# Optimization experiments

Measured on AMD Instinct MI355X. Metric: run time of the kernel, lower is better.

The kernel has to match this reference:

```python
import jax, jax.numpy as jnp
import numpy as np

N_CLI, N_AGG, E, D, L = 100000, 1000, 1600000, 128, 3


def setup_inputs() -> dict:
    key = jax.random.key(0)
    ks = jax.random.split(key, 16)
    inp = {
        'x_clients': jax.random.normal(ks[0], (N_CLI, D), jnp.float32),
        'x_agg': jax.random.normal(ks[1], (N_AGG, D), jnp.float32),
        'c2a_src': jax.random.randint(ks[2], (E,), 0, N_CLI, jnp.int32),
        'c2a_dst': jax.random.randint(ks[3], (E,), 0, N_AGG, jnp.int32),
        'a2c_src': jax.random.randint(ks[4], (E,), 0, N_AGG, jnp.int32),
        'a2c_dst': jax.random.randint(ks[5], (E,), 0, N_CLI, jnp.int32),
    }
    s = 1.0 / np.sqrt(D)
    # stacked per-layer SAGE params for each edge type: W_l (on aggregated msg), W_r (on dst), b
    inp['Wl_c2a'] = jax.random.uniform(ks[6], (L, D, D), jnp.float32, -s, s)
    inp['Wr_c2a'] = jax.random.uniform(ks[7], (L, D, D), jnp.float32, -s, s)
    inp['b_c2a'] = jax.random.uniform(ks[8], (L, D), jnp.float32, -s, s)
    inp['Wl_a2c'] = jax.random.uniform(ks[9], (L, D, D), jnp.float32, -s, s)
    inp['Wr_a2c'] = jax.random.uniform(ks[10], (L, D, D), jnp.float32, -s, s)
    inp['b_a2c'] = jax.random.uniform(ks[11], (L, D), jnp.float32, -s, s)
    inp['W_lin'] = jax.random.uniform(ks[12], (D, 1), jnp.float32, -s, s)
    inp['b_lin'] = jax.random.uniform(ks[13], (1,), jnp.float32, -s, s)
    return inp


def _sage(x_src, x_dst, src, dst, Wl, Wr, b, n_dst):
    # mean aggregation of gathered source features onto dst nodes
    msg = x_src[src]                                        # [E, D]
    summed = jax.ops.segment_sum(msg, dst, num_segments=n_dst)
    cnt = jax.ops.segment_sum(jnp.ones((src.shape[0], 1), x_src.dtype), dst, num_segments=n_dst)
    mean = summed / jnp.maximum(cnt, 1.0)
    return mean @ Wl + x_dst @ Wr + b


def _leaky(x):
    return jnp.where(x >= 0, x, 0.1 * x)


def reference(x_clients, x_agg, c2a_src, c2a_dst, a2c_src, a2c_dst,
              Wl_c2a, Wr_c2a, b_c2a, Wl_a2c, Wr_a2c, b_a2c, W_lin, b_lin):
    xc, xa = x_clients, x_agg
    for l in range(L):
        new_a = _sage(xc, xa, c2a_src, c2a_dst, Wl_c2a[l], Wr_c2a[l], b_c2a[l], N_AGG)
        new_c = _sage(xa, xc, a2c_src, a2c_dst, Wl_a2c[l], Wr_a2c[l], b_a2c[l], N_CLI)
        xa, xc = _leaky(new_a), _leaky(new_c)
    return (xc @ W_lin + b_lin).squeeze(1)
```

## Files before the change

### kernel.cpp

```cpp
#include <hip/hip_runtime.h>

#define D      128
#define NCLI   100000
#define NAGG   1000
#define NLAYER 3
#define NBKT   782
#define NRNG   8
#define NBIN   (NAGG * NRNG)
#define RMAGIC 343598u
#define NHIST  512
#define NCVTX  (NCLI * D / 4 / 256)
#define NCVTW  ((NLAYER * D * D + 255) / 256)
#define NROWT  (NCLI / 32)

typedef short bf16x8 __attribute__((ext_vector_type(8)));
typedef float f32x16 __attribute__((ext_vector_type(16)));

static __device__ __forceinline__ float leaky(float x) { return x >= 0.f ? x : 0.1f * x; }

static __device__ __forceinline__ unsigned bf16_rn(float f) {
    unsigned u = __float_as_uint(f);
    return (u + 0x7fffu + ((u >> 16) & 1u)) >> 16;
}
static __device__ __forceinline__ float bf_val(unsigned h) { return __uint_as_float(h << 16); }
static __device__ __forceinline__ unsigned pack_bf2(float lo, float hi) {
    return bf16_rn(lo) | (bf16_rn(hi) << 16);
}
static __device__ __forceinline__ float bf_lo(unsigned v) { return __uint_as_float(v << 16); }
static __device__ __forceinline__ float bf_hi(unsigned v) { return __uint_as_float(v & 0xffff0000u); }

__global__ __launch_bounds__(256) void prep(const int* __restrict__ c2a_src,
                                            const int* __restrict__ c2a_dst,
                                            const int* __restrict__ a2c_dst, int E,
                                            int* __restrict__ cnt_ar, int* __restrict__ bcnt,
                                            const float4* __restrict__ X4,
                                            uint2* __restrict__ xhi, uint2* __restrict__ xlo,
                                            const float* __restrict__ W,
                                            unsigned short* __restrict__ Wt) {
    __shared__ int h[NBIN + NBKT];
    int bid = blockIdx.x;
    if (bid < NHIST) {
        for (int i = threadIdx.x; i < NBIN + NBKT; i += 256) h[i] = 0;
        __syncthreads();
        int stride = NHIST * 256;
        for (int e = bid * 256 + threadIdx.x; e < E; e += stride) {
            int s = c2a_src[e];
            int bin = c2a_dst[e] * NRNG + (int)__umulhi((unsigned)s, RMAGIC);
            atomicAdd(&h[bin], 1);
            atomicAdd(&h[NBIN + (a2c_dst[e] >> 7)], 1);
        }
        __syncthreads();
        for (int i = threadIdx.x; i < NBIN; i += 256)
            if (h[i]) atomicAdd(&cnt_ar[i], h[i]);
        for (int i = threadIdx.x; i < NBKT; i += 256)
            if (h[NBIN + i]) atomicAdd(&bcnt[i], h[NBIN + i]);
    } else if (bid < NHIST + NCVTX) {
        int t = (bid - NHIST) * 256 + threadIdx.x;
        float4 f = X4[t];
        unsigned h0 = bf16_rn(f.x), h1 = bf16_rn(f.y), h2 = bf16_rn(f.z), h3 = bf16_rn(f.w);
        xhi[t] = make_uint2(h0 | (h1 << 16), h2 | (h3 << 16));
        xlo[t] = make_uint2(pack_bf2(f.x - bf_val(h0), f.y - bf_val(h1)),
                            pack_bf2(f.z - bf_val(h2), f.w - bf_val(h3)));
    } else {
        int idx = (bid - NHIST - NCVTX) * 256 + threadIdx.x;
        if (idx >= NLAYER * D * D) return;
        int layer = idx >> 14, rem = idx & (D * D - 1);
        int k = rem >> 7, n = rem & 127;
        float w = W[layer * D * D + k * D + n];
        unsigned hh = bf16_rn(w);
        unsigned short* base = Wt + layer * 2 * D * D;
        base[n * D + k] = (unsigned short)hh;
        base[D * D + n * D + k] = (unsigned short)bf16_rn(w - bf_val(hh));
    }
}

__global__ void scan_both(const int* __restrict__ cnt_ar, int* __restrict__ rp_ar,
                          int* __restrict__ cur_ar, const int* __restrict__ bcnt,
                          int* __restrict__ brp, int* __restrict__ bcur) {
    __shared__ int sh[1024];
    int t = threadIdx.x;
    if (blockIdx.x == 0) {
        int v[8];
        int s = 0;
#pragma unroll
        for (int j = 0; j < 8; j++) {
            int idx = t * 8 + j;
            v[j] = (idx < NBIN) ? cnt_ar[idx] : 0;
            s += v[j];
        }
        sh[t] = s;
        __syncthreads();
        for (int off = 1; off < 1024; off <<= 1) {
            int x = (t >= off) ? sh[t - off] : 0;
            __syncthreads();
            sh[t] += x;
            __syncthreads();
        }
        int run = sh[t] - s;
#pragma unroll
        for (int j = 0; j < 8; j++) {
            int idx = t * 8 + j;
            if (idx < NBIN) {
                rp_ar[idx] = run;
                cur_ar[idx] = run;
            }
            run += v[j];
        }
        if (t == 1023) rp_ar[NBIN] = sh[1023];
    } else {
        int v = (t < NBKT) ? bcnt[t] : 0;
        sh[t] = v;
        __syncthreads();
        for (int off = 1; off < 1024; off <<= 1) {
            int x = (t >= off) ? sh[t - off] : 0;
            __syncthreads();
            sh[t] += x;
            __syncthreads();
        }
        if (t == 0) { brp[0] = 0; bcur[0] = 0; }
        if (t < NBKT) {
            brp[t + 1] = sh[t];
            if (t + 1 < NBKT) bcur[t + 1] = sh[t];
        }
    }
}

__global__ __launch_bounds__(1024) void scatter_both(const int* __restrict__ c2a_src,
                                                     const int* __restrict__ c2a_dst,
                                                     const int* __restrict__ a2c_src,
                                                     const int* __restrict__ a2c_dst, int E,
                                                     int* __restrict__ cur_ar,
                                                     int* __restrict__ col_c2a,
                                                     int* __restrict__ bcur,
                                                     int* __restrict__ sorted1) {
    __shared__ int sbuf[2 * NBIN];
    int tid = threadIdx.x;
    if (blockIdx.x < 256) {
        int* h = sbuf;
        int* base = sbuf + NBIN;
        int chunk = (E + 255) / 256;
        int e0 = blockIdx.x * chunk;
        int e1 = min(E, e0 + chunk);
        for (int i = tid; i < NBIN; i += 1024) h[i] = 0;
        __syncthreads();
        for (int e = e0 + tid; e < e1; e += 1024) {
            int s = c2a_src[e];
            atomicAdd(&h[c2a_dst[e] * NRNG + (int)__umulhi((unsigned)s, RMAGIC)], 1);
        }
        __syncthreads();
        for (int i = tid; i < NBIN; i += 1024) {
            int c = h[i];
            base[i] = c ? atomicAdd(&cur_ar[i], c) : 0;
        }
        __syncthreads();
        for (int e = e0 + tid; e < e1; e += 1024) {
            int s = c2a_src[e];
            int bin = c2a_dst[e] * NRNG + (int)__umulhi((unsigned)s, RMAGIC);
            int pos = atomicAdd(&base[bin], 1);
            col_c2a[pos] = s;
        }
    } else {
        int* h = sbuf;
        int* base = sbuf + NBKT;
        int bid = blockIdx.x - 256;
        int chunk = (E + 255) / 256;
        int e0 = bid * chunk;
        int e1 = min(E, e0 + chunk);
        for (int i = tid; i < NBKT; i += 1024) h[i] = 0;
        __syncthreads();
        for (int e = e0 + tid; e < e1; e += 1024) atomicAdd(&h[a2c_dst[e] >> 7], 1);
        __syncthreads();
        for (int i = tid; i < NBKT; i += 1024) {
            int c = h[i];
            base[i] = c ? atomicAdd(&bcur[i], c) : 0;
        }
        __syncthreads();
        for (int e = e0 + tid; e < e1; e += 1024) {
            int d = a2c_dst[e];
            int pos = atomicAdd(&base[d >> 7], 1);
            sorted1[pos] = ((d & 127) << 10) | a2c_src[e];
        }
    }
}

__global__ __launch_bounds__(512) void bucket_csr(const int* __restrict__ brp,
                                                  const int* __restrict__ sorted1,
                                                  int* __restrict__ rp_c,
                                                  int* __restrict__ col) {
    __shared__ int h[128], cur[128];
    int b = blockIdx.x, tid = threadIdx.x;
    if (tid < 128) h[tid] = 0;
    __syncthreads();
    int beg = brp[b], end = brp[b + 1];
    for (int e = beg + tid; e < end; e += 512) atomicAdd(&h[sorted1[e] >> 10], 1);
    __syncthreads();
    if (tid < 128) cur[tid] = h[tid];
    __syncthreads();
    for (int off = 1; off < 128; off <<= 1) {
        int x = 0;
        if (tid < 128 && tid >= off) x = cur[tid - off];
        __syncthreads();
        if (tid < 128) cur[tid] += x;
        __syncthreads();
    }
    if (tid < 128) {
        int start = beg + cur[tid] - h[tid];
        int c = b * 128 + tid;
        if (c < NCLI) rp_c[c] = start;
        cur[tid] = start;
    }
    if (b == NBKT - 1 && tid == 0) rp_c[NCLI] = end;
    __syncthreads();
    for (int e = beg + tid; e < end; e += 512) {
        int p = sorted1[e];
        int pos = atomicAdd(&cur[p >> 10], 1);
        col[pos] = p & 1023;
    }
}


__global__ __launch_bounds__(512) void gather_mean(const unsigned* __restrict__ tbl,
                                                   const int* __restrict__ rp_ar,
                                                   const int* __restrict__ col,
                                                   float* __restrict__ psum) {
    __shared__ float part[4][8][D];
    int quad = blockIdx.x >> 3, r = blockIdx.x & 7;
    int tid = threadIdx.x;
    int a = tid >> 7;
    int sub = (tid >> 4) & 7;
    int sl = tid & 15;
    const uint4* tbl4 = (const uint4*)tbl;
    int agg = quad * 4 + a;
    int bin = agg * NRNG + r;
    int beg = rp_ar[bin], end = rp_ar[bin + 1];
    float f0 = 0, f1 = 0, f2 = 0, f3 = 0, f4 = 0, f5 = 0, f6 = 0, f7 = 0;
    int e = beg + sub;
    for (; e + 8 < end; e += 16) {
        int s0 = col[e];
        int s1 = col[e + 8];
        uint4 v0 = tbl4[(s0 << 4) + sl];
        uint4 v1 = tbl4[(s1 << 4) + sl];
        f0 += bf_lo(v0.x); f1 += bf_hi(v0.x); f2 += bf_lo(v0.y); f3 += bf_hi(v0.y);
        f4 += bf_lo(v0.z); f5 += bf_hi(v0.z); f6 += bf_lo(v0.w); f7 += bf_hi(v0.w);
        f0 += bf_lo(v1.x); f1 += bf_hi(v1.x); f2 += bf_lo(v1.y); f3 += bf_hi(v1.y);
        f4 += bf_lo(v1.z); f5 += bf_hi(v1.z); f6 += bf_lo(v1.w); f7 += bf_hi(v1.w);
    }
    if (e < end) {
        int s0 = col[e];
        uint4 v0 = tbl4[(s0 << 4) + sl];
        f0 += bf_lo(v0.x); f1 += bf_hi(v0.x); f2 += bf_lo(v0.y); f3 += bf_hi(v0.y);
        f4 += bf_lo(v0.z); f5 += bf_hi(v0.z); f6 += bf_lo(v0.w); f7 += bf_hi(v0.w);
    }
    float* pr = &part[a][sub][sl * 8];
    pr[0] = f0; pr[1] = f1; pr[2] = f2; pr[3] = f3;
    pr[4] = f4; pr[5] = f5; pr[6] = f6; pr[7] = f7;
    __syncthreads();
    int c = tid & 127;
    float s = 0.f;
#pragma unroll
    for (int g = 0; g < 8; g++) s += part[a][g][c];
    psum[((size_t)agg * NRNG + r) * D + c] = s;
}

__global__ __launch_bounds__(128) void combine_agg(const float* __restrict__ psum,
                                                   const int* __restrict__ rp_ar,
                                                   const float* xa_old,
                                                   const float* __restrict__ Wl_a2c,
                                                   const float* __restrict__ Wl_c2a,
                                                   const float* __restrict__ Wr_c2a,
                                                   const float* __restrict__ b_c2a,
                                                   unsigned short* __restrict__ ya_bf,
                                                   float* xa_out) {
    __shared__ float mr[D], xr[D];
    int i = blockIdx.x, j = threadIdx.x;
    const float* pr = psum + (size_t)i * NRNG * D + j;
    float s = 0.f;
#pragma unroll
    for (int r = 0; r < NRNG; r++) s += pr[r * D];
    int deg = rp_ar[i * NRNG + NRNG] - rp_ar[i * NRNG];
    mr[j] = s / fmaxf((float)deg, 1.f);
    xr[j] = xa_old[i * D + j];
    __syncthreads();
    float accy = 0.f, accn = b_c2a[j];
#pragma unroll 4
    for (int k = 0; k < D; k++) {
        accy += xr[k] * Wl_a2c[k * D + j];
        accn += mr[k] * Wl_c2a[k * D + j] + xr[k] * Wr_c2a[k * D + j];
    }
    ya_bf[i * D + j] = (unsigned short)bf16_rn(accy);
    xa_out[i * D + j] = leaky(accn);
}

__global__ __launch_bounds__(256) void gemm_mfma(const unsigned short* __restrict__ Ahi,
                                                 const unsigned short* __restrict__ Alo,
                                                 const unsigned short* __restrict__ Wt,
                                                 const float* __restrict__ bias,
                                                 float* __restrict__ Y) {
    int tid = threadIdx.x;
    int wave = tid >> 6, lane = tid & 63;
    int cl = lane & 31, kh = lane >> 5;
    int n0 = wave * 32;
    const unsigned short* Wlo = Wt + D * D;
    const unsigned short* wbh = Wt + (size_t)(n0 + cl) * D + kh * 8;
    const unsigned short* wbl = Wlo + (size_t)(n0 + cl) * D + kh * 8;
    bf16x8 bhi[8], blo[8];
#pragma unroll
    for (int kc = 0; kc < 8; kc++) {
        bhi[kc] = *(const bf16x8*)(wbh + kc * 16);
        blo[kc] = *(const bf16x8*)(wbl + kc * 16);
    }
    float bv = bias[n0 + cl];
    for (int r = blockIdx.x; r < NROWT; r += gridDim.x) {
        int m0 = r * 32;
        const unsigned short* ar = Ahi + (size_t)(m0 + cl) * D + kh * 8;
        const unsigned short* al = Alo + (size_t)(m0 + cl) * D + kh * 8;
        bf16x8 ahi[8], alo[8];
#pragma unroll
        for (int kc = 0; kc < 8; kc++) {
            ahi[kc] = *(const bf16x8*)(ar + kc * 16);
            alo[kc] = *(const bf16x8*)(al + kc * 16);
        }
        f32x16 acc;
#pragma unroll
        for (int q = 0; q < 16; q++) acc[q] = bv;
#pragma unroll
        for (int kc = 0; kc < 8; kc++) {
            acc = __builtin_amdgcn_mfma_f32_32x32x16_bf16(ahi[kc], bhi[kc], acc, 0, 0, 0);
            acc = __builtin_amdgcn_mfma_f32_32x32x16_bf16(alo[kc], bhi[kc], acc, 0, 0, 0);
            acc = __builtin_amdgcn_mfma_f32_32x32x16_bf16(ahi[kc], blo[kc], acc, 0, 0, 0);
        }
        float* yb = Y + (size_t)m0 * D + n0 + cl;
#pragma unroll
        for (int reg = 0; reg < 16; reg++) {
            int row = (reg & 3) + 8 * (reg >> 2) + 4 * kh;
            yb[(size_t)row * D] = acc[reg];
        }
    }
}

template <int LAST>
__global__ __launch_bounds__(256) void agg_c_bf(const unsigned* __restrict__ ya,
                                                const int* __restrict__ rowptr,
                                                const int* __restrict__ col,
                                                const float* __restrict__ Y,
                                                unsigned* __restrict__ xhi,
                                                unsigned* __restrict__ xlo,
                                                const float* __restrict__ Wlin,
                                                const float* __restrict__ blin,
                                                float* __restrict__ out, int E) {
    int l = threadIdx.x & 63;
    int gid = blockIdx.x * 4 + (threadIdx.x >> 6);
    if (gid >= NCLI) return;
    int beg = rowptr[gid], end = rowptr[gid + 1];
    float a0 = 0, b0 = 0, a1 = 0, b1 = 0, a2 = 0, b2 = 0, a3 = 0, b3 = 0;
    float a4 = 0, b4 = 0, a5 = 0, b5 = 0, a6 = 0, b6 = 0, a7 = 0, b7 = 0;
    for (int ch = beg; ch < end; ch += 64) {
        int len = min(64, end - ch);
        int ec = col[min(ch + l, E - 1)];
        int j = 0;
        for (; j + 8 <= len; j += 8) {
            int r0 = __shfl(ec, j + 0), r1 = __shfl(ec, j + 1);
            int r2 = __shfl(ec, j + 2), r3 = __shfl(ec, j + 3);
            int r4 = __shfl(ec, j + 4), r5 = __shfl(ec, j + 5);
            int r6 = __shfl(ec, j + 6), r7 = __shfl(ec, j + 7);
            unsigned v0 = ya[(r0 << 6) + l];
            unsigned v1 = ya[(r1 << 6) + l];
            unsigned v2 = ya[(r2 << 6) + l];
            unsigned v3 = ya[(r3 << 6) + l];
            unsigned v4 = ya[(r4 << 6) + l];
            unsigned v5 = ya[(r5 << 6) + l];
            unsigned v6 = ya[(r6 << 6) + l];
            unsigned v7 = ya[(r7 << 6) + l];
            a0 += bf_lo(v0); b0 += bf_hi(v0);
            a1 += bf_lo(v1); b1 += bf_hi(v1);
            a2 += bf_lo(v2); b2 += bf_hi(v2);
            a3 += bf_lo(v3); b3 += bf_hi(v3);
            a4 += bf_lo(v4); b4 += bf_hi(v4);
            a5 += bf_lo(v5); b5 += bf_hi(v5);
            a6 += bf_lo(v6); b6 += bf_hi(v6);
            a7 += bf_lo(v7); b7 += bf_hi(v7);
        }
        for (; j < len; j++) {
            int r = __shfl(ec, j);
            unsigned v = ya[(r << 6) + l];
            a0 += bf_lo(v); b0 += bf_hi(v);
        }
    }
    float sx = ((a0 + a1) + (a2 + a3)) + ((a4 + a5) + (a6 + a7));
    float sy = ((b0 + b1) + (b2 + b3)) + ((b4 + b5) + (b6 + b7));
    float inv = 1.f / fmaxf((float)(end - beg), 1.f);
    float2 yv = *(const float2*)&Y[(size_t)gid * D + 2 * l];
    float r0 = leaky(yv.x + sx * inv);
    float r1 = leaky(yv.y + sy * inv);
    if (LAST) {
        float2 w = *(const float2*)&Wlin[2 * l];
        float v = r0 * w.x + r1 * w.y;
#pragma unroll
        for (int off = 32; off > 0; off >>= 1) v += __shfl_down(v, off);
        if (l == 0) out[gid] = v + blin[0];
    } else {
        unsigned h0 = bf16_rn(r0), h1 = bf16_rn(r1);
        xhi[(gid << 6) + l] = h0 | (h1 << 16);
        xlo[(gid << 6) + l] = pack_bf2(r0 - bf_val(h0), r1 - bf_val(h1));
    }
}

extern "C" void kernel_launch(void* const* d_in, const int* in_sizes, int n_in,
                              void* d_out, int out_size, void* d_ws, size_t ws_size,
                              hipStream_t stream) {
    const float* x_clients = (const float*)d_in[0];
    const float* x_agg     = (const float*)d_in[1];
    const int*   c2a_src   = (const int*)d_in[2];
    const int*   c2a_dst   = (const int*)d_in[3];
    const int*   a2c_src   = (const int*)d_in[4];
    const int*   a2c_dst   = (const int*)d_in[5];
    const float* Wl_c2a    = (const float*)d_in[6];
    const float* Wr_c2a    = (const float*)d_in[7];
    const float* b_c2a     = (const float*)d_in[8];
    const float* Wl_a2c    = (const float*)d_in[9];
    const float* Wr_a2c    = (const float*)d_in[10];
    const float* b_a2c     = (const float*)d_in[11];
    const float* W_lin     = (const float*)d_in[12];
    const float* b_lin     = (const float*)d_in[13];
    float* out = (float*)d_out;
    const int E = in_sizes[2];

    char* p = (char*)d_ws;
    auto alloc = [&](size_t bytes) {
        char* r = p;
        p += (bytes + 255) & ~(size_t)255;
        return r;
    };
    float*    Yb    = (float*)alloc(sizeof(float) * NCLI * D);
    unsigned* xc_hi = (unsigned*)alloc(sizeof(unsigned) * NCLI * 64);
    unsigned* xc_lo = (unsigned*)alloc(sizeof(unsigned) * NCLI * 64);
    float*    xa    = (float*)alloc(sizeof(float) * NAGG * D);
    unsigned short* ya_bf = (unsigned short*)alloc(sizeof(unsigned short) * NAGG * D);
    unsigned short* Wt = (unsigned short*)alloc(sizeof(unsigned short) * NLAYER * 2 * D * D);
    float* psum  = (float*)alloc(sizeof(float) * NAGG * NRNG * D);
    int* cnt_ar = (int*)alloc(sizeof(int) * (NBIN + NBKT));
    int* bcnt  = cnt_ar + NBIN;
    int* rp_ar = (int*)alloc(sizeof(int) * (NBIN + 1));
    int* cur_ar = (int*)alloc(sizeof(int) * NBIN);
    int* brp   = (int*)alloc(sizeof(int) * (NBKT + 1));
    int* bcur  = (int*)alloc(sizeof(int) * NBKT);
    int* rp_c  = (int*)alloc(sizeof(int) * (NCLI + 1));
    int* col_c2a = (int*)alloc(sizeof(int) * E);
    int* col_a2c = (int*)alloc(sizeof(int) * E);
    int* sorted1 = (int*)Yb;

    hipMemsetAsync(cnt_ar, 0, sizeof(int) * (NBIN + NBKT), stream);

    prep<<<NHIST + NCVTX + NCVTW, 256, 0, stream>>>(c2a_src, c2a_dst, a2c_dst, E, cnt_ar, bcnt,
                                                    (const float4*)x_clients,
                                                    (uint2*)xc_hi, (uint2*)xc_lo,
                                                    Wr_a2c, Wt);
    scan_both<<<2, 1024, 0, stream>>>(cnt_ar, rp_ar, cur_ar, bcnt, brp, bcur);
    scatter_both<<<512, 1024, 0, stream>>>(c2a_src, c2a_dst, a2c_src, a2c_dst, E,
                                           cur_ar, col_c2a, bcur, sorted1);
    bucket_csr<<<NBKT, 512, 0, stream>>>(brp, sorted1, rp_c, col_a2c);

    const float* xa_old = x_agg;
    for (int l = 0; l < NLAYER; l++) {
        gather_mean<<<(NAGG / 4) * NRNG, 512, 0, stream>>>(xc_hi, rp_ar, col_c2a, psum);
        combine_agg<<<NAGG, 128, 0, stream>>>(psum, rp_ar, xa_old,
                                              Wl_a2c + l * D * D, Wl_c2a + l * D * D,
                                              Wr_c2a + l * D * D, b_c2a + l * D, ya_bf, xa);
        gemm_mfma<<<625, 256, 0, stream>>>(
            (const unsigned short*)xc_hi, (const unsigned short*)xc_lo,
            Wt + l * 2 * D * D, b_a2c + l * D, Yb);
        if (l < NLAYER - 1) {
            agg_c_bf<0><<<(NCLI + 3) / 4, 256, 0, stream>>>((const unsigned*)ya_bf, rp_c, col_a2c,
                                                            Yb, xc_hi, xc_lo, nullptr, nullptr,
                                                            nullptr, E);
        } else {
            agg_c_bf<1><<<(NCLI + 3) / 4, 256, 0, stream>>>((const unsigned*)ya_bf, rp_c, col_a2c,
                                                            Yb, nullptr, nullptr, W_lin, b_lin,
                                                            out, E);
        }
        xa_old = xa;
    }
}
```

Measured before the change: 633.8 us.

## Build c2a CSR with two-pass radix scatter, range-major bins

Reorders the c2a bin layout to range-major (range * NAGG + agg). CSR construction becomes a two-pass scatter: first a wave-ballot partition of edges into 8 source ranges, then a per-range scatter by destination using small shared histograms. This replaces the single scatter over 8000 bins, which needed large shared memory and gave poor locality, and folds the a2c bucket CSR pass into the second kernel. The cost is an extra pass over a packed intermediate buffer placed in Yb, plus an 8-term degree sum in combine_agg.

```diff
diff --git a/kernel.cpp b/kernel.cpp
--- a/kernel.cpp
+++ b/kernel.cpp
@@ -45,7 +45,7 @@
         int stride = NHIST * 256;
         for (int e = bid * 256 + threadIdx.x; e < E; e += stride) {
             int s = c2a_src[e];
-            int bin = c2a_dst[e] * NRNG + (int)__umulhi((unsigned)s, RMAGIC);
+            int bin = (int)__umulhi((unsigned)s, RMAGIC) * NAGG + c2a_dst[e];
             atomicAdd(&h[bin], 1);
             atomicAdd(&h[NBIN + (a2c_dst[e] >> 7)], 1);
         }
@@ -75,7 +75,8 @@
 }
 
 __global__ void scan_both(const int* __restrict__ cnt_ar, int* __restrict__ rp_ar,
-                          int* __restrict__ cur_ar, const int* __restrict__ bcnt,
+                          int* __restrict__ cur_ar, int* __restrict__ cur_r8,
+                          const int* __restrict__ bcnt,
                           int* __restrict__ brp, int* __restrict__ bcur) {
     __shared__ int sh[1024];
     int t = threadIdx.x;
@@ -103,6 +104,7 @@
             if (idx < NBIN) {
                 rp_ar[idx] = run;
                 cur_ar[idx] = run;
+                if ((idx % NAGG) == 0) cur_r8[idx / NAGG] = run;
             }
             run += v[j];
         }
@@ -125,44 +127,61 @@
     }
 }
 
-__global__ __launch_bounds__(1024) void scatter_both(const int* __restrict__ c2a_src,
-                                                     const int* __restrict__ c2a_dst,
-                                                     const int* __restrict__ a2c_src,
-                                                     const int* __restrict__ a2c_dst, int E,
-                                                     int* __restrict__ cur_ar,
-                                                     int* __restrict__ col_c2a,
-                                                     int* __restrict__ bcur,
-                                                     int* __restrict__ sorted1) {
-    __shared__ int sbuf[2 * NBIN];
+__global__ __launch_bounds__(1024) void scatter1(const int* __restrict__ c2a_src,
+                                                 const int* __restrict__ c2a_dst,
+                                                 const int* __restrict__ a2c_src,
+                                                 const int* __restrict__ a2c_dst, int E,
+                                                 int* __restrict__ cur_r8,
+                                                 int* __restrict__ sorted_c2a,
+                                                 int* __restrict__ bcur,
+                                                 int* __restrict__ sorted1) {
+    __shared__ int sbuf[2 * NBKT];
     int tid = threadIdx.x;
-    if (blockIdx.x < 256) {
+    if (blockIdx.x < 64) {
         int* h = sbuf;
-        int* base = sbuf + NBIN;
-        int chunk = (E + 255) / 256;
+        int* base = sbuf + 8;
+        int chunk = (E + 63) / 64;
         int e0 = blockIdx.x * chunk;
         int e1 = min(E, e0 + chunk);
-        for (int i = tid; i < NBIN; i += 1024) h[i] = 0;
-        __syncthreads();
-        for (int e = e0 + tid; e < e1; e += 1024) {
-            int s = c2a_src[e];
-            atomicAdd(&h[c2a_dst[e] * NRNG + (int)__umulhi((unsigned)s, RMAGIC)], 1);
-        }
-        __syncthreads();
-        for (int i = tid; i < NBIN; i += 1024) {
-            int c = h[i];
-            base[i] = c ? atomicAdd(&cur_ar[i], c) : 0;
-        }
-        __syncthreads();
-        for (int e = e0 + tid; e < e1; e += 1024) {
-            int s = c2a_src[e];
-            int bin = c2a_dst[e] * NRNG + (int)__umulhi((unsigned)s, RMAGIC);
-            int pos = atomicAdd(&base[bin], 1);
-            col_c2a[pos] = s;
+        int wid = tid >> 6, lane = tid & 63;
+        unsigned long long below = (1ull << lane) - 1;
+        if (tid < 8) h[tid] = 0;
+        __syncthreads();
+        for (int eb = e0 + wid * 64; eb < e1; eb += 16 * 64) {
+            int e = eb + lane;
+            bool valid = e < e1;
+            int s = valid ? c2a_src[e] : 0;
+            int rg = (int)__umulhi((unsigned)s, RMAGIC);
+#pragma unroll
+            for (int r = 0; r < NRNG; r++) {
+                unsigned long long m = __ballot(valid && rg == r);
+                if (lane == r && m) atomicAdd(&h[r], __popcll(m));
+            }
+        }
+        __syncthreads();
+        if (tid < 8) base[tid] = h[tid] ? atomicAdd(&cur_r8[tid], h[tid]) : 0;
+        __syncthreads();
+        for (int eb = e0 + wid * 64; eb < e1; eb += 16 * 64) {
+            int e = eb + lane;
+            bool valid = e < e1;
+            int s = valid ? c2a_src[e] : 0;
+            int dcl = valid ? c2a_dst[e] : 0;
+            int rg = (int)__umulhi((unsigned)s, RMAGIC);
+            unsigned long long mym = 0;
+            int wb = 0;
+#pragma unroll
+            for (int r = 0; r < NRNG; r++) {
+                unsigned long long m = __ballot(valid && rg == r);
+                if (valid && rg == r) mym = m;
+                if (lane == r) wb = m ? atomicAdd(&base[r], __popcll(m)) : 0;
+            }
+            int pb = __shfl(wb, rg);
+            if (valid) sorted_c2a[pb + __popcll(mym & below)] = (dcl << 17) | s;
         }
     } else {
         int* h = sbuf;
         int* base = sbuf + NBKT;
-        int bid = blockIdx.x - 256;
+        int bid = blockIdx.x - 64;
         int chunk = (E + 255) / 256;
         int e0 = bid * chunk;
         int e1 = min(E, e0 + chunk);
@@ -183,38 +202,70 @@
     }
 }
 
-__global__ __launch_bounds__(512) void bucket_csr(const int* __restrict__ brp,
-                                                  const int* __restrict__ sorted1,
-                                                  int* __restrict__ rp_c,
-                                                  int* __restrict__ col) {
-    __shared__ int h[128], cur[128];
-    int b = blockIdx.x, tid = threadIdx.x;
-    if (tid < 128) h[tid] = 0;
-    __syncthreads();
-    int beg = brp[b], end = brp[b + 1];
-    for (int e = beg + tid; e < end; e += 512) atomicAdd(&h[sorted1[e] >> 10], 1);
-    __syncthreads();
-    if (tid < 128) cur[tid] = h[tid];
-    __syncthreads();
-    for (int off = 1; off < 128; off <<= 1) {
-        int x = 0;
-        if (tid < 128 && tid >= off) x = cur[tid - off];
-        __syncthreads();
-        if (tid < 128) cur[tid] += x;
-        __syncthreads();
-    }
-    if (tid < 128) {
-        int start = beg + cur[tid] - h[tid];
-        int c = b * 128 + tid;
-        if (c < NCLI) rp_c[c] = start;
-        cur[tid] = start;
-    }
-    if (b == NBKT - 1 && tid == 0) rp_c[NCLI] = end;
-    __syncthreads();
-    for (int e = beg + tid; e < end; e += 512) {
-        int p = sorted1[e];
-        int pos = atomicAdd(&cur[p >> 10], 1);
-        col[pos] = p & 1023;
+__global__ __launch_bounds__(1024) void scatter2(const int* __restrict__ sorted_c2a,
+                                                 const int* __restrict__ rp_ar,
+                                                 int* __restrict__ cur_ar,
+                                                 int* __restrict__ col_c2a, int E,
+                                                 const int* __restrict__ brp,
+                                                 const int* __restrict__ sorted1,
+                                                 int* __restrict__ rp_c,
+                                                 int* __restrict__ col_a2c) {
+    __shared__ int sb[2 * NAGG];
+    int tid = threadIdx.x;
+    if (blockIdx.x < 256) {
+        int* h = sb;
+        int* base = sb + NAGG;
+        int r = blockIdx.x >> 5, k = blockIdx.x & 31;
+        int seg0 = rp_ar[r * NAGG];
+        int seg1 = rp_ar[(r + 1) * NAGG];
+        int chunk = (seg1 - seg0 + 31) / 32;
+        int e0 = seg0 + k * chunk;
+        int e1 = min(seg1, e0 + chunk);
+        for (int i = tid; i < NAGG; i += 1024) h[i] = 0;
+        __syncthreads();
+        for (int e = e0 + tid; e < e1; e += 1024) atomicAdd(&h[sorted_c2a[e] >> 17], 1);
+        __syncthreads();
+        for (int i = tid; i < NAGG; i += 1024) {
+            int c = h[i];
+            base[i] = c ? atomicAdd(&cur_ar[r * NAGG + i], c) : 0;
+        }
+        __syncthreads();
+        for (int e = e0 + tid; e < e1; e += 1024) {
+            int p = sorted_c2a[e];
+            int pos = atomicAdd(&base[p >> 17], 1);
+            col_c2a[pos] = p & 0x1FFFF;
+        }
+    } else {
+        int* h = sb;
+        int* cur = sb + 128;
+        int b = blockIdx.x - 256;
+        if (tid < 128) h[tid] = 0;
+        __syncthreads();
+        int beg = brp[b], end = brp[b + 1];
+        for (int e = beg + tid; e < end; e += 1024) atomicAdd(&h[sorted1[e] >> 10], 1);
+        __syncthreads();
+        if (tid < 128) cur[tid] = h[tid];
+        __syncthreads();
+        for (int off = 1; off < 128; off <<= 1) {
+            int x = 0;
+            if (tid < 128 && tid >= off) x = cur[tid - off];
+            __syncthreads();
+            if (tid < 128) cur[tid] += x;
+            __syncthreads();
+        }
+        if (tid < 128) {
+            int start = beg + cur[tid] - h[tid];
+            int c = b * 128 + tid;
+            if (c < NCLI) rp_c[c] = start;
+            cur[tid] = start;
+        }
+        if (b == NBKT - 1 && tid == 0) rp_c[NCLI] = end;
+        __syncthreads();
+        for (int e = beg + tid; e < end; e += 1024) {
+            int p = sorted1[e];
+            int pos = atomicAdd(&cur[p >> 10], 1);
+            col_a2c[pos] = p & 1023;
+        }
     }
 }
 
@@ -231,7 +282,7 @@
     int sl = tid & 15;
     const uint4* tbl4 = (const uint4*)tbl;
     int agg = quad * 4 + a;
-    int bin = agg * NRNG + r;
+    int bin = r * NAGG + agg;
     int beg = rp_ar[bin], end = rp_ar[bin + 1];
     float f0 = 0, f1 = 0, f2 = 0, f3 = 0, f4 = 0, f5 = 0, f6 = 0, f7 = 0;
     int e = beg + sub;
@@ -277,7 +328,9 @@
     float s = 0.f;
 #pragma unroll
     for (int r = 0; r < NRNG; r++) s += pr[r * D];
-    int deg = rp_ar[i * NRNG + NRNG] - rp_ar[i * NRNG];
+    int deg = 0;
+#pragma unroll
+    for (int r = 0; r < NRNG; r++) deg += rp_ar[r * NAGG + i + 1] - rp_ar[r * NAGG + i];
     mr[j] = s / fmaxf((float)deg, 1.f);
     xr[j] = xa_old[i * D + j];
     __syncthreads();
@@ -442,12 +495,14 @@
     int* bcnt  = cnt_ar + NBIN;
     int* rp_ar = (int*)alloc(sizeof(int) * (NBIN + 1));
     int* cur_ar = (int*)alloc(sizeof(int) * NBIN);
+    int* cur_r8 = (int*)alloc(sizeof(int) * NRNG);
     int* brp   = (int*)alloc(sizeof(int) * (NBKT + 1));
     int* bcur  = (int*)alloc(sizeof(int) * NBKT);
     int* rp_c  = (int*)alloc(sizeof(int) * (NCLI + 1));
     int* col_c2a = (int*)alloc(sizeof(int) * E);
     int* col_a2c = (int*)alloc(sizeof(int) * E);
-    int* sorted1 = (int*)Yb;
+    int* sorted1    = (int*)Yb;
+    int* sorted_c2a = sorted1 + E;
 
     hipMemsetAsync(cnt_ar, 0, sizeof(int) * (NBIN + NBKT), stream);
 
@@ -455,10 +510,11 @@
                                                     (const float4*)x_clients,
                                                     (uint2*)xc_hi, (uint2*)xc_lo,
                                                     Wr_a2c, Wt);
-    scan_both<<<2, 1024, 0, stream>>>(cnt_ar, rp_ar, cur_ar, bcnt, brp, bcur);
-    scatter_both<<<512, 1024, 0, stream>>>(c2a_src, c2a_dst, a2c_src, a2c_dst, E,
-                                           cur_ar, col_c2a, bcur, sorted1);
-    bucket_csr<<<NBKT, 512, 0, stream>>>(brp, sorted1, rp_c, col_a2c);
+    scan_both<<<2, 1024, 0, stream>>>(cnt_ar, rp_ar, cur_ar, cur_r8, bcnt, brp, bcur);
+    scatter1<<<320, 1024, 0, stream>>>(c2a_src, c2a_dst, a2c_src, a2c_dst, E,
+                                       cur_r8, sorted_c2a, bcur, sorted1);
+    scatter2<<<256 + NBKT, 1024, 0, stream>>>(sorted_c2a, rp_ar, cur_ar, col_c2a, E,
+                                              brp, sorted1, rp_c, col_a2c);
 
     const float* xa_old = x_agg;
     for (int l = 0; l < NLAYER; l++) {
```

Result: slower. 646.7 us (+2.0%).
